# Kernel tuning notes

Hardware: AMD Instinct MI355X
Metric: run time of the kernel (lower is better)

Reference implementation:

```python
import jax, jax.numpy as jnp
import numpy as np

D_MODEL = 1024
NHEAD = 16
HEAD_DIM = D_MODEL // NHEAD


def setup_inputs() -> dict:
    key = jax.random.key(0)
    k1, k2, k3 = jax.random.split(key, 3)
    x = jax.random.normal(k1, (4, 2048, D_MODEL), dtype=jnp.float32)
    # xavier_uniform init for weights, zero bias
    lim_qkv = float(np.sqrt(6.0 / (D_MODEL + 3 * D_MODEL)))
    w_qkv = jax.random.uniform(k2, (3 * D_MODEL, D_MODEL), jnp.float32, -lim_qkv, lim_qkv)
    b_qkv = jnp.zeros((3 * D_MODEL,), jnp.float32)
    lim_o = float(np.sqrt(6.0 / (D_MODEL + D_MODEL)))
    w_o = jax.random.uniform(k3, (D_MODEL, D_MODEL), jnp.float32, -lim_o, lim_o)
    b_o = jnp.zeros((D_MODEL,), jnp.float32)
    return {"x": x, "w_qkv": w_qkv, "b_qkv": b_qkv, "w_o": w_o, "b_o": b_o}


def reference(x, w_qkv, b_qkv, w_o, b_o):
    B, S, _ = x.shape
    qkv = x @ w_qkv.T + b_qkv                      # [B,S,3D]
    qkv = qkv.reshape(B, S, NHEAD, 3 * HEAD_DIM).transpose(0, 2, 1, 3)  # [B,H,S,3d]
    q, k, v = jnp.split(qkv, 3, axis=-1)           # each [B,H,S,d]
    scale = 1.0 / jnp.sqrt(jnp.asarray(HEAD_DIM, x.dtype))
    logits = jnp.einsum('bhqd,bhkd->bhqk', q, k) * scale
    attn = jax.nn.softmax(logits, axis=-1)
    vals = jnp.einsum('bhqk,bhkd->bhqd', attn, v)  # [B,H,S,d]
    vals = vals.transpose(0, 2, 1, 3).reshape(B, S, D_MODEL)
    return vals @ w_o.T + b_o
```

## Files before the change

kernel.cpp:

```cpp
#include <hip/hip_runtime.h>
#include <hip/hip_bf16.h>
#include <stdint.h>

typedef unsigned short u16;
typedef __bf16 bf16x8 __attribute__((ext_vector_type(8)));
typedef short s16x4 __attribute__((ext_vector_type(4)));
typedef float f32x4 __attribute__((ext_vector_type(4)));
typedef u16 u16x4v __attribute__((ext_vector_type(4)));

#define AS1 __attribute__((address_space(1)))
#define AS3 __attribute__((address_space(3)))

__device__ __forceinline__ void gld_lds16(const u16* g, u16* l) {
    __builtin_amdgcn_global_load_lds((const AS1 uint32_t*)g, (AS3 uint32_t*)l, 16, 0, 0);
}

__device__ __forceinline__ u16 f2bf(float f) {
    union { float f; uint32_t u; } v; v.f = f;
    uint32_t u = v.u;
    return (u16)((u + 0x7FFFu + ((u >> 16) & 1u)) >> 16);
}

#define QSCALE 0.18033688011112042f

__global__ void cast_f32_bf16(const float* __restrict__ in, u16* __restrict__ out, int n4) {
    int i = blockIdx.x * blockDim.x + threadIdx.x;
    if (i < n4) {
        float4 f = ((const float4*)in)[i];
        u16x4v o;
        o.x = f2bf(f.x); o.y = f2bf(f.y); o.z = f2bf(f.z); o.w = f2bf(f.w);
        ((u16x4v*)out)[i] = o;
    }
}

template <int OUT_BF16, int PRESCALE_Q>
__global__ __launch_bounds__(256, 2) void gemm_bt(
    const u16* __restrict__ A, const u16* __restrict__ B,
    const float* __restrict__ bias, void* __restrict__ Cout,
    int K, int ldc)
{
    __shared__ __align__(16) u16 As[128 * 32];
    __shared__ __align__(16) u16 Bs[128 * 32];
    const int tid = threadIdx.x;
    const int lane = tid & 63;
    const int w = tid >> 6;
    const int wm = (w >> 1) << 6;
    const int wn = (w & 1) << 6;
    const int r = lane & 15;
    const int q = lane >> 4;
    const int m0 = blockIdx.y << 7;
    const int n0 = blockIdx.x << 7;

    const f32x4 zero4 = {0.f, 0.f, 0.f, 0.f};
    f32x4 acc[4][4];
#pragma unroll
    for (int i = 0; i < 4; ++i)
#pragma unroll
        for (int j = 0; j < 4; ++j) acc[i][j] = zero4;

    const int nk = K >> 5;
    for (int kt = 0; kt < nk; ++kt) {
        const int kk = kt << 5;
#pragma unroll
        for (int p = 0; p < 2; ++p) {
            const int idx = (p << 8) + tid;
            const int row = idx >> 2;
            const int cg = ((idx & 3) - (row >> 1)) & 3;
            gld_lds16(A + (m0 + row) * K + kk + (cg << 3), &As[idx << 3]);
            gld_lds16(B + (n0 + row) * K + kk + (cg << 3), &Bs[idx << 3]);
        }
        __syncthreads();
        bf16x8 af[4], bf[4];
#pragma unroll
        for (int i = 0; i < 4; ++i) {
            const int ra = wm + (i << 4) + r;
            af[i] = *(const bf16x8*)&As[((ra << 2) + ((q + (ra >> 1)) & 3)) << 3];
            const int rb = wn + (i << 4) + r;
            bf[i] = *(const bf16x8*)&Bs[((rb << 2) + ((q + (rb >> 1)) & 3)) << 3];
        }
#pragma unroll
        for (int i = 0; i < 4; ++i)
#pragma unroll
            for (int j = 0; j < 4; ++j)
                acc[i][j] = __builtin_amdgcn_mfma_f32_16x16x32_bf16(af[i], bf[j], acc[i][j], 0, 0, 0);
        __syncthreads();
    }

#pragma unroll
    for (int j = 0; j < 4; ++j) {
        const int col = n0 + wn + (j << 4) + r;
        const float bv = bias[col];
        float scl = 1.0f;
        if (PRESCALE_Q) scl = ((col % 192) < 64) ? QSCALE : 1.0f;
#pragma unroll
        for (int i = 0; i < 4; ++i) {
#pragma unroll
            for (int ii = 0; ii < 4; ++ii) {
                const int rowg = m0 + wm + (i << 4) + (q << 2) + ii;
                const float v = (acc[i][j][ii] + bv) * scl;
                if (OUT_BF16) ((u16*)Cout)[rowg * ldc + col] = f2bf(v);
                else          ((float*)Cout)[rowg * ldc + col] = v;
            }
        }
    }
}

__global__ __launch_bounds__(256, 4) void attn(const u16* __restrict__ qkv, u16* __restrict__ vals)
{
    __shared__ __align__(16) u16 Qs[128 * 64];
    __shared__ __align__(16) u16 Ks[64 * 64];
    __shared__ __align__(16) u16 VTs[64 * 64];

    const int tid = threadIdx.x;
    const int lane = tid & 63;
    const int w = tid >> 6;
    const int r = lane & 15;
    const int q = lane >> 4;
    const int q0 = blockIdx.x << 7;
    const int h = blockIdx.y;
    const int b = blockIdx.z;
    const size_t base = ((size_t)b * 2048) * 3072 + h * 192;

#pragma unroll
    for (int p = 0; p < 4; ++p) {
        const int idx = (p << 8) + tid;
        const int row = idx >> 3;
        const int cg = ((idx & 7) - row) & 7;
        gld_lds16(qkv + base + (size_t)(q0 + row) * 3072 + (cg << 3), &Qs[idx << 3]);
    }

    const f32x4 zero4 = {0.f, 0.f, 0.f, 0.f};
    f32x4 oacc[4][2];
    float lpart[2];
#pragma unroll
    for (int ht = 0; ht < 4; ++ht)
#pragma unroll
        for (int nt = 0; nt < 2; ++nt) oacc[ht][nt] = zero4;
    lpart[0] = 0.f; lpart[1] = 0.f;

    for (int kt = 0; kt < 32; ++kt) {
        const int k0 = kt << 6;
#pragma unroll
        for (int p = 0; p < 2; ++p) {
            const int idx = (p << 8) + tid;
            const int row = idx >> 3;
            const int cg = ((idx & 7) - row) & 7;
            gld_lds16(qkv + base + 64 + (size_t)(k0 + row) * 3072 + (cg << 3), &Ks[idx << 3]);
        }
#pragma unroll
        for (int p = 0; p < 2; ++p) {
            const int idx = (p << 8) + tid;
            const int vrow = idx >> 3;
            const int c8 = idx & 7;
            union { uint4 u; u16 s[8]; } d;
            d.u = *(const uint4*)(qkv + base + 128 + (size_t)(k0 + vrow) * 3072 + (c8 << 3));
#pragma unroll
            for (int j = 0; j < 8; ++j) {
                const int hd = (c8 << 3) + j;
                const int pc = ((vrow >> 3) + hd + (hd >> 3)) & 7;
                VTs[(hd << 6) + (pc << 3) + (vrow & 7)] = d.s[j];
            }
        }
        __syncthreads();

        f32x4 sacc[4][2];
#pragma unroll
        for (int mt = 0; mt < 4; ++mt)
#pragma unroll
            for (int nt = 0; nt < 2; ++nt) sacc[mt][nt] = zero4;
#pragma unroll
        for (int ks = 0; ks < 2; ++ks) {
            const int L = (ks << 2) + q;
            bf16x8 bq[2], ak[4];
#pragma unroll
            for (int nt = 0; nt < 2; ++nt) {
                const int row = (w << 5) + (nt << 4) + r;
                bq[nt] = *(const bf16x8*)&Qs[(row << 6) + (((L + row) & 7) << 3)];
            }
#pragma unroll
            for (int mt = 0; mt < 4; ++mt) {
                const int row = (mt << 4) + r;
                ak[mt] = *(const bf16x8*)&Ks[(row << 6) + (((L + row) & 7) << 3)];
            }
#pragma unroll
            for (int mt = 0; mt < 4; ++mt)
#pragma unroll
                for (int nt = 0; nt < 2; ++nt)
                    sacc[mt][nt] = __builtin_amdgcn_mfma_f32_16x16x32_bf16(ak[mt], bq[nt], sacc[mt][nt], 0, 0, 0);
        }

        s16x4 pb[4][2];
#pragma unroll
        for (int mt = 0; mt < 4; ++mt) {
#pragma unroll
            for (int nt = 0; nt < 2; ++nt) {
                const float e0 = __builtin_amdgcn_exp2f(sacc[mt][nt][0]);
                const float e1 = __builtin_amdgcn_exp2f(sacc[mt][nt][1]);
                const float e2 = __builtin_amdgcn_exp2f(sacc[mt][nt][2]);
                const float e3 = __builtin_amdgcn_exp2f(sacc[mt][nt][3]);
                lpart[nt] += (e0 + e1) + (e2 + e3);
                union { __hip_bfloat162 h2[2]; s16x4 v; } u;
                u.h2[0] = __float22bfloat162_rn(float2{e0, e1});
                u.h2[1] = __float22bfloat162_rn(float2{e2, e3});
                pb[mt][nt] = u.v;
            }
        }

#pragma unroll
        for (int mt = 0; mt < 4; ++mt) {
            s16x4 av[4];
#pragma unroll
            for (int ht = 0; ht < 4; ++ht) {
                const int hd = (ht << 4) + r;
                const int chunk = (mt << 1) + (q >> 1);
                const int pc = (chunk + hd + (hd >> 3)) & 7;
                av[ht] = *(const s16x4*)&VTs[(hd << 6) + (pc << 3) + ((q & 1) << 2)];
            }
#pragma unroll
            for (int ht = 0; ht < 4; ++ht)
#pragma unroll
                for (int nt = 0; nt < 2; ++nt)
                    oacc[ht][nt] = __builtin_amdgcn_mfma_f32_16x16x16bf16_1k(av[ht], pb[mt][nt], oacc[ht][nt], 0, 0, 0);
        }
        __syncthreads();
    }

#pragma unroll
    for (int nt = 0; nt < 2; ++nt) {
        float l = lpart[nt];
        l += __shfl_xor(l, 16, 64);
        l += __shfl_xor(l, 32, 64);
        const float inv = 1.f / l;
        const int srow = q0 + (w << 5) + (nt << 4) + r;
#pragma unroll
        for (int ht = 0; ht < 4; ++ht) {
            u16x4v vv;
            vv.x = f2bf(oacc[ht][nt][0] * inv);
            vv.y = f2bf(oacc[ht][nt][1] * inv);
            vv.z = f2bf(oacc[ht][nt][2] * inv);
            vv.w = f2bf(oacc[ht][nt][3] * inv);
            const int col = (h << 6) + (ht << 4) + (q << 2);
            *(u16x4v*)&vals[((size_t)b * 2048 + srow) * 1024 + col] = vv;
        }
    }
}

extern "C" void kernel_launch(void* const* d_in, const int* in_sizes, int n_in,
                              void* d_out, int out_size, void* d_ws, size_t ws_size,
                              hipStream_t stream) {
    (void)in_sizes; (void)n_in; (void)out_size; (void)ws_size;
    const float* x     = (const float*)d_in[0];
    const float* w_qkv = (const float*)d_in[1];
    const float* b_qkv = (const float*)d_in[2];
    const float* w_o   = (const float*)d_in[3];
    const float* b_o   = (const float*)d_in[4];
    float* out = (float*)d_out;

    char* ws = (char*)d_ws;
    u16* xb    = (u16*)(ws);
    u16* wqkvb = (u16*)(ws + (size_t)(16 << 20));
    u16* wob   = (u16*)(ws + (size_t)(22 << 20));
    u16* qkvb  = (u16*)(ws + (size_t)(24 << 20));
    u16* valsb = (u16*)(ws + (size_t)(72 << 20));

    cast_f32_bf16<<<8192, 256, 0, stream>>>(x, xb, 2097152);
    cast_f32_bf16<<<3072, 256, 0, stream>>>(w_qkv, wqkvb, 786432);
    cast_f32_bf16<<<1024, 256, 0, stream>>>(w_o, wob, 262144);

    gemm_bt<1, 1><<<dim3(24, 64), 256, 0, stream>>>(xb, wqkvb, b_qkv, (void*)qkvb, 1024, 3072);

    attn<<<dim3(16, 16, 4), 256, 0, stream>>>(qkvb, valsb);

    gemm_bt<0, 0><<<dim3(8, 64), 256, 0, stream>>>(valsb, wob, b_o, (void*)out, 1024, 1024);
}
```

Measured before the change: 302.2 us.

## Split QKV into separate Q/K buffers and pre-transposed V from GEMM epilogue

The QKV projection epilogue now writes Q (prescaled), K and a transposed V into separate bf16 buffers instead of one interleaved [B,S,3D] tensor. The attention kernel can then stream V^T into LDS with direct global-to-LDS loads instead of per-element scalar scatter transposes in every key tile. The grid mapping is also swapped so that head varies fastest across blocks, which may change L2 reuse of K/V. In exchange, the GEMM epilogue does strided transposed stores for V, which may cost write efficiency.

```diff
diff --git a/kernel.cpp b/kernel.cpp
--- a/kernel.cpp
+++ b/kernel.cpp
@@ -33,10 +33,11 @@
     }
 }
 
-template <int OUT_BF16, int PRESCALE_Q>
+template <int MODE>
 __global__ __launch_bounds__(256, 2) void gemm_bt(
     const u16* __restrict__ A, const u16* __restrict__ B,
-    const float* __restrict__ bias, void* __restrict__ Cout,
+    const float* __restrict__ bias, float* __restrict__ Cf,
+    u16* __restrict__ qb, u16* __restrict__ kb, u16* __restrict__ vT,
     int K, int ldc)
 {
     __shared__ __align__(16) u16 As[128 * 32];
@@ -90,22 +91,55 @@
     for (int j = 0; j < 4; ++j) {
         const int col = n0 + wn + (j << 4) + r;
         const float bv = bias[col];
-        float scl = 1.0f;
-        if (PRESCALE_Q) scl = ((col % 192) < 64) ? QSCALE : 1.0f;
-#pragma unroll
-        for (int i = 0; i < 4; ++i) {
-#pragma unroll
-            for (int ii = 0; ii < 4; ++ii) {
-                const int rowg = m0 + wm + (i << 4) + (q << 2) + ii;
-                const float v = (acc[i][j][ii] + bv) * scl;
-                if (OUT_BF16) ((u16*)Cout)[rowg * ldc + col] = f2bf(v);
-                else          ((float*)Cout)[rowg * ldc + col] = v;
-            }
-        }
-    }
-}
-
-__global__ __launch_bounds__(256, 4) void attn(const u16* __restrict__ qkv, u16* __restrict__ vals)
+        if (MODE == 0) {
+#pragma unroll
+            for (int i = 0; i < 4; ++i)
+#pragma unroll
+                for (int ii = 0; ii < 4; ++ii) {
+                    const int rowg = m0 + wm + (i << 4) + (q << 2) + ii;
+                    Cf[rowg * ldc + col] = acc[i][j][ii] + bv;
+                }
+        } else {
+            const int c0 = n0 + wn + (j << 4);
+            const int h = c0 / 192;
+            const int rem = c0 - h * 192;
+            const int region = rem >> 6;
+            const int colp = (h << 6) + (rem - (region << 6)) + r;
+            if (region == 0) {
+#pragma unroll
+                for (int i = 0; i < 4; ++i)
+#pragma unroll
+                    for (int ii = 0; ii < 4; ++ii) {
+                        const int rowg = m0 + wm + (i << 4) + (q << 2) + ii;
+                        qb[rowg * 1024 + colp] = f2bf((acc[i][j][ii] + bv) * QSCALE);
+                    }
+            } else if (region == 1) {
+#pragma unroll
+                for (int i = 0; i < 4; ++i)
+#pragma unroll
+                    for (int ii = 0; ii < 4; ++ii) {
+                        const int rowg = m0 + wm + (i << 4) + (q << 2) + ii;
+                        kb[rowg * 1024 + colp] = f2bf(acc[i][j][ii] + bv);
+                    }
+            } else {
+#pragma unroll
+                for (int i = 0; i < 4; ++i) {
+                    const int rowg0 = m0 + wm + (i << 4) + (q << 2);
+                    u16x4v vv;
+                    vv.x = f2bf(acc[i][j][0] + bv);
+                    vv.y = f2bf(acc[i][j][1] + bv);
+                    vv.z = f2bf(acc[i][j][2] + bv);
+                    vv.w = f2bf(acc[i][j][3] + bv);
+                    *(u16x4v*)&vT[(size_t)colp * 8192 + rowg0] = vv;
+                }
+            }
+        }
+    }
+}
+
+__global__ __launch_bounds__(256, 4) void attn(
+    const u16* __restrict__ qb, const u16* __restrict__ kb,
+    const u16* __restrict__ vT, u16* __restrict__ vals)
 {
     __shared__ __align__(16) u16 Qs[128 * 64];
     __shared__ __align__(16) u16 Ks[64 * 64];
@@ -116,17 +150,17 @@
     const int w = tid >> 6;
     const int r = lane & 15;
     const int q = lane >> 4;
-    const int q0 = blockIdx.x << 7;
-    const int h = blockIdx.y;
+    const int h = blockIdx.x;
+    const int q0 = blockIdx.y << 7;
     const int b = blockIdx.z;
-    const size_t base = ((size_t)b * 2048) * 3072 + h * 192;
+    const size_t rowbase = (size_t)b * 2048;
 
 #pragma unroll
     for (int p = 0; p < 4; ++p) {
         const int idx = (p << 8) + tid;
         const int row = idx >> 3;
         const int cg = ((idx & 7) - row) & 7;
-        gld_lds16(qkv + base + (size_t)(q0 + row) * 3072 + (cg << 3), &Qs[idx << 3]);
+        gld_lds16(qb + (rowbase + q0 + row) * 1024 + (h << 6) + (cg << 3), &Qs[idx << 3]);
     }
 
     const f32x4 zero4 = {0.f, 0.f, 0.f, 0.f};
@@ -145,21 +179,15 @@
             const int idx = (p << 8) + tid;
             const int row = idx >> 3;
             const int cg = ((idx & 7) - row) & 7;
-            gld_lds16(qkv + base + 64 + (size_t)(k0 + row) * 3072 + (cg << 3), &Ks[idx << 3]);
+            gld_lds16(kb + (rowbase + k0 + row) * 1024 + (h << 6) + (cg << 3), &Ks[idx << 3]);
         }
 #pragma unroll
         for (int p = 0; p < 2; ++p) {
             const int idx = (p << 8) + tid;
-            const int vrow = idx >> 3;
-            const int c8 = idx & 7;
-            union { uint4 u; u16 s[8]; } d;
-            d.u = *(const uint4*)(qkv + base + 128 + (size_t)(k0 + vrow) * 3072 + (c8 << 3));
-#pragma unroll
-            for (int j = 0; j < 8; ++j) {
-                const int hd = (c8 << 3) + j;
-                const int pc = ((vrow >> 3) + hd + (hd >> 3)) & 7;
-                VTs[(hd << 6) + (pc << 3) + (vrow & 7)] = d.s[j];
-            }
+            const int hd = idx >> 3;
+            const int pc = idx & 7;
+            const int lc = (pc - hd - (hd >> 3)) & 7;
+            gld_lds16(vT + (size_t)((h << 6) + hd) * 8192 + rowbase + k0 + (lc << 3), &VTs[idx << 3]);
         }
         __syncthreads();
 
@@ -240,7 +268,7 @@
             vv.z = f2bf(oacc[ht][nt][2] * inv);
             vv.w = f2bf(oacc[ht][nt][3] * inv);
             const int col = (h << 6) + (ht << 4) + (q << 2);
-            *(u16x4v*)&vals[((size_t)b * 2048 + srow) * 1024 + col] = vv;
+            *(u16x4v*)&vals[(rowbase + srow) * 1024 + col] = vv;
         }
     }
 }
@@ -260,16 +288,20 @@
     u16* xb    = (u16*)(ws);
     u16* wqkvb = (u16*)(ws + (size_t)(16 << 20));
     u16* wob   = (u16*)(ws + (size_t)(22 << 20));
-    u16* qkvb  = (u16*)(ws + (size_t)(24 << 20));
+    u16* qb    = (u16*)(ws + (size_t)(24 << 20));
+    u16* kb    = (u16*)(ws + (size_t)(40 << 20));
+    u16* vTb   = (u16*)(ws + (size_t)(56 << 20));
     u16* valsb = (u16*)(ws + (size_t)(72 << 20));
 
     cast_f32_bf16<<<8192, 256, 0, stream>>>(x, xb, 2097152);
     cast_f32_bf16<<<3072, 256, 0, stream>>>(w_qkv, wqkvb, 786432);
     cast_f32_bf16<<<1024, 256, 0, stream>>>(w_o, wob, 262144);
 
-    gemm_bt<1, 1><<<dim3(24, 64), 256, 0, stream>>>(xb, wqkvb, b_qkv, (void*)qkvb, 1024, 3072);
-
-    attn<<<dim3(16, 16, 4), 256, 0, stream>>>(qkvb, valsb);
-
-    gemm_bt<0, 0><<<dim3(8, 64), 256, 0, stream>>>(valsb, wob, b_o, (void*)out, 1024, 1024);
-}
+    gemm_bt<1><<<dim3(24, 64), 256, 0, stream>>>(xb, wqkvb, b_qkv, nullptr,
+                                                 qb, kb, vTb, 1024, 3072);
+
+    attn<<<dim3(16, 16, 4), 256, 0, stream>>>(qb, kb, vTb, valsb);
+
+    gemm_bt<0><<<dim3(8, 64), 256, 0, stream>>>(valsb, wob, b_o, out,
+                                                nullptr, nullptr, nullptr, 1024, 1024);
+}
```

New measurement: 290.2 us. -4.0%, faster.
